# Kernel tuning notes

Measured on AMD Instinct MI355X. Metric: run time of the kernel, lower is better.

The kernel has to match this reference:

```python
import jax, jax.numpy as jnp
import numpy as np

B, S, D_IN = 32, 128, 17
D_PT, D_PAIR, D_OUT = 64, 128, 64
EPS = 1e-5


def _gelu(x):
    return jax.nn.gelu(x, approximate=False)  # torch nn.GELU default (erf)


def _bn(h, g, b):
    # BatchNorm1d (training mode): stats over batch and pair dims, per channel
    mean = h.mean(axis=(0, 1))
    var = h.var(axis=(0, 1))  # biased, matching torch normalization
    return (h - mean) * jax.lax.rsqrt(var + EPS) * g + b


def setup_inputs() -> dict:
    key = jax.random.key(0)
    ks = jax.random.split(key, 8)
    s = lambda k, shp, fan: jax.random.normal(k, shp, jnp.float32) * (1.0 / np.sqrt(fan))
    return {
        "x": jax.random.normal(ks[0], (B, S, D_IN), jnp.float32),
        # pointwise MLP: 17 -> 64 -> 64
        "w1": s(ks[1], (D_IN, D_PT), D_IN), "b1": jnp.zeros((D_PT,), jnp.float32),
        "w2": s(ks[2], (D_PT, D_PT), D_PT), "b2": jnp.zeros((D_PT,), jnp.float32),
        # pair MLP: 128 -> 128 -> 128 (input = 2 * D_PT)
        "wp1": s(ks[3], (2 * D_PT, D_PAIR), 2 * D_PT), "bp1": jnp.zeros((D_PAIR,), jnp.float32),
        "wp2": s(ks[4], (D_PAIR, D_PAIR), D_PAIR), "bp2": jnp.zeros((D_PAIR,), jnp.float32),
        # embed: BN(128) -> Conv1d(128,64,1) -> BN(64) -> GELU -> Conv1d(64,64,1) -> BN(64)
        "g0": jnp.ones((D_PAIR,), jnp.float32), "be0": jnp.zeros((D_PAIR,), jnp.float32),
        "wc1": s(ks[5], (D_PAIR, D_OUT), D_PAIR), "bc1": jnp.zeros((D_OUT,), jnp.float32),
        "g1": jnp.ones((D_OUT,), jnp.float32), "be1": jnp.zeros((D_OUT,), jnp.float32),
        "wc2": s(ks[6], (D_OUT, D_OUT), D_OUT), "bc2": jnp.zeros((D_OUT,), jnp.float32),
        "g2": jnp.ones((D_OUT,), jnp.float32), "be2": jnp.zeros((D_OUT,), jnp.float32),
    }


def reference(x, w1, b1, w2, b2, wp1, bp1, wp2, bp2,
              g0, be0, wc1, bc1, g1, be1, wc2, bc2, g2, be2):
    seq_len = x.shape[1]
    # pointwise MLP
    h = _gelu(x @ w1 + b1)
    h = _gelu(h @ w2 + b2)  # [B, S, D_PT]
    # tril pair gather (xi = features of particle j, xj = of particle i,
    # matching x_rep[b, a, c] = x[b, c] semantics in the torch code)
    i_idx, j_idx = jnp.tril_indices(seq_len)
    xi = h[:, j_idx, :]  # [B, P, D_PT]
    xj = h[:, i_idx, :]
    xij = jnp.concatenate([xi, xj], axis=-1)  # [B, P, 2*D_PT]
    # pair MLP
    e = _gelu(xij @ wp1 + bp1)
    e = _gelu(e @ wp2 + bp2)  # [B, P, D_PAIR]
    # embed stack (Conv1d k=1 == channel-wise linear)
    e = _bn(e, g0, be0)
    e = _gelu(_bn(e @ wc1 + bc1, g1, be1))
    e = _bn(e @ wc2 + bc2, g2, be2)  # [B, P, D_OUT]
    # symmetric scatter into dense pairwise output
    y = jnp.zeros((x.shape[0], seq_len, seq_len, e.shape[-1]), e.dtype)
    y = y.at[:, i_idx, j_idx, :].set(e)
    y = y.at[:, j_idx, i_idx, :].set(e)
    return y
```

## Files before the change

kernel.cpp:

```cpp
#include <hip/hip_runtime.h>
#include <hip/hip_bf16.h>
#include <math.h>

#define BB 32
#define SS 128
#define DIN 17
#define DPT 64
#define DPA 128
#define DOU 64
#define NP 8256
#define NROWS (BB * NP)
#define NCHUNK (NROWS / 128)
#define EPSF 1e-5f

typedef __hip_bfloat16 bf16;
typedef __attribute__((ext_vector_type(8))) short short8;
typedef __attribute__((ext_vector_type(16))) float f32x16;
typedef __attribute__((ext_vector_type(4))) float f32x4;
typedef __attribute__((ext_vector_type(4))) unsigned int uint4v;

#define MFMA32(a, b, c) __builtin_amdgcn_mfma_f32_32x32x16_bf16(a, b, c, 0, 0, 0)

__device__ __forceinline__ float bf2f(short u) {
    return __builtin_bit_cast(float, ((unsigned int)(unsigned short)u) << 16);
}

__device__ __forceinline__ void plswap(unsigned int& a, unsigned int& b) {
    asm("v_permlane32_swap_b32 %0, %1" : "+v"(a), "+v"(b));
}
__device__ __forceinline__ unsigned int cvtpk(float lo, float hi) {
    unsigned int r;
    asm("v_cvt_pk_bf16_f32 %0, %1, %2" : "=v"(r) : "v"(lo), "v"(hi));
    return r;
}

__device__ __forceinline__ void xform(const f32x16& a, short8& o0, short8& o1) {
    unsigned int w[8];
#pragma unroll
    for (int j = 0; j < 8; ++j) w[j] = cvtpk(a[2 * j], a[2 * j + 1]);
    plswap(w[0], w[2]);
    plswap(w[1], w[3]);
    plswap(w[4], w[6]);
    plswap(w[5], w[7]);
    uint4v u0 = {w[0], w[1], w[2], w[3]};
    uint4v u1 = {w[4], w[5], w[6], w[7]};
    o0 = __builtin_bit_cast(short8, u0);
    o1 = __builtin_bit_cast(short8, u1);
}

__device__ __forceinline__ float gelu_exact(float x) {
    float x2 = x * x;
    float m = fmaf(0.0356774081f, x2, 0.7978845608f);
    float e = __expf(2.0f * x * m);
    float r = __builtin_amdgcn_rcpf(e + 1.0f);
    return fmaf(-x, r, x);
}
__device__ __forceinline__ void gelu16(f32x16& a) {
#pragma unroll
    for (int r = 0; r < 16; ++r) a[r] = gelu_exact(a[r]);
}

__global__ void k_pairs(int* __restrict__ pairIJ) {
    int p = blockIdx.x * blockDim.x + threadIdx.x;
    if (p >= NP) return;
    int i = (int)((sqrtf(8.0f * (float)p + 1.0f) - 1.0f) * 0.5f);
    while ((i * (i + 1)) / 2 > p) --i;
    while (((i + 1) * (i + 2)) / 2 <= p) ++i;
    int j = p - (i * (i + 1)) / 2;
    pairIJ[p] = (i << 8) | j;
}

__global__ void k_pack(const float* __restrict__ wp2, const float* __restrict__ wc2,
                       bf16* __restrict__ fragP2, bf16* __restrict__ fragC2) {
    int id = blockIdx.x * 256 + threadIdx.x;
    if (id < 16384) {
        int f = id >> 9, lane = (id >> 3) & 63, i = id & 7;
        int mt = f >> 3, s = f & 7;
        int k = s * 16 + (lane >> 5) * 8 + i;
        int m = mt * 32 + (lane & 31);
        fragP2[id] = __float2bfloat16(wp2[k * DPA + m]);
    } else if (id < 20480) {
        int rem = id - 16384;
        int f = rem >> 9, lane = (rem >> 3) & 63, i = rem & 7;
        int mt = f >> 2, s = f & 3;
        int k = s * 16 + (lane >> 5) * 8 + i;
        int m = mt * 32 + (lane & 31);
        fragC2[rem] = __float2bfloat16(wc2[k * DOU + m]);
    }
}

__global__ void k_fold(const float* __restrict__ a0, const float* __restrict__ d0,
                       const float* __restrict__ wc1, const float* __restrict__ bc1,
                       bf16* __restrict__ fragC1, float* __restrict__ bc1p) {
    int id = blockIdx.x * 256 + threadIdx.x;
    if (id < 8192) {
        int f = id >> 9, lane = (id >> 3) & 63, i = id & 7;
        int mt = f >> 3, s = f & 7;
        int k = s * 16 + (lane >> 5) * 8 + i;
        int m = mt * 32 + (lane & 31);
        fragC1[id] = __float2bfloat16(a0[k] * wc1[k * DOU + m]);
    } else if (id < 8192 + 64) {
        int c = id - 8192;
        float s = bc1[c];
        for (int k = 0; k < DPA; ++k) s = fmaf(d0[k], wc1[k * DOU + c], s);
        bc1p[c] = s;
    }
}

__global__ __launch_bounds__(256) void k_h(
    const float* __restrict__ x, const float* __restrict__ w1,
    const float* __restrict__ b1, const float* __restrict__ w2,
    const float* __restrict__ b2, const float* __restrict__ wp1,
    const float* __restrict__ bp1, bf16* __restrict__ u, bf16* __restrict__ v) {
    __shared__ float h1[4][DPT];
    __shared__ float h2[4][DPT];
    __shared__ float wt[128][64];
    int t = threadIdx.x;
    int rs = t >> 6, c = t & 63;
    int r = blockIdx.x * 4 + rs;
    const float* xr = x + (size_t)r * DIN;
    float acc = b1[c];
#pragma unroll
    for (int k = 0; k < DIN; ++k) acc += xr[k] * w1[k * DPT + c];
    h1[rs][c] = gelu_exact(acc);
    __syncthreads();
    float acc2 = b2[c];
#pragma unroll
    for (int k = 0; k < DPT; ++k) acc2 += h1[rs][k] * w2[k * DPT + c];
    h2[rs][c] = gelu_exact(acc2);

    for (int cp = 0; cp < 2; ++cp) {
        __syncthreads();
        for (int idx = t; idx < 8192; idx += 256) {
            int k = idx >> 6, cc = idx & 63;
            wt[k][cc] = wp1[k * DPA + cp * 64 + cc];
        }
        __syncthreads();
        float au = bp1[cp * 64 + c], av = 0.f;
#pragma unroll
        for (int k = 0; k < 64; ++k) {
            float hk = h2[rs][k];
            au = fmaf(hk, wt[k][c], au);
            av = fmaf(hk, wt[64 + k][c], av);
        }
        u[(size_t)r * DPA + cp * 64 + c] = __float2bfloat16(au);
        v[(size_t)r * DPA + cp * 64 + c] = __float2bfloat16(av);
    }
}

__global__ __launch_bounds__(256, 3) void k_e0m(
    const bf16* __restrict__ u, const bf16* __restrict__ v,
    const int* __restrict__ pairIJ, const short8* __restrict__ fragP2,
    const float* __restrict__ bp2, bf16* __restrict__ e0,
    float* __restrict__ part) {
    __shared__ __align__(16) char lds[32768];
    int t = threadIdx.x;
    int w = t >> 6, l = t & 63;
    int l31 = l & 31, lhi = l >> 5;
    int row0 = blockIdx.x * 128;
    int prow = w * 32 + l31;

    for (int uq = t; uq < 2048; uq += 256)
        *(short8*)(lds + uq * 16) = fragP2[uq];

    int n = row0 + prow;
    int b = n / NP, p = n - b * NP;
    int ij = pairIJ[p];
    const bf16* ur = u + (((size_t)(b * SS + (ij & 255))) << 7);
    const bf16* vr = v + (((size_t)(b * SS + (ij >> 8))) << 7);
    short8 B2[8];
#pragma unroll
    for (int s = 0; s < 8; ++s) {
        short8 us = *(const short8*)(ur + s * 16 + lhi * 8);
        short8 vs = *(const short8*)(vr + s * 16 + lhi * 8);
        float g[8];
#pragma unroll
        for (int i = 0; i < 8; ++i)
            g[i] = gelu_exact(bf2f(us[i]) + bf2f(vs[i]));
        uint4v pk = {cvtpk(g[0], g[1]), cvtpk(g[2], g[3]),
                     cvtpk(g[4], g[5]), cvtpk(g[6], g[7])};
        B2[s] = __builtin_bit_cast(short8, pk);
    }
    __syncthreads();

    short8 o[8];
#pragma unroll
    for (int mp = 0; mp < 2; ++mp) {
        f32x16 c0, c1;
#pragma unroll
        for (int g = 0; g < 4; ++g) {
            f32x4 v0 = *(const f32x4*)(bp2 + (2 * mp) * 32 + g * 8 + lhi * 4);
            f32x4 v1 = *(const f32x4*)(bp2 + (2 * mp + 1) * 32 + g * 8 + lhi * 4);
#pragma unroll
            for (int j = 0; j < 4; ++j) { c0[g * 4 + j] = v0[j]; c1[g * 4 + j] = v1[j]; }
        }
#pragma unroll
        for (int s = 0; s < 8; ++s) {
            short8 a0 = *(const short8*)(lds + (((2 * mp) * 8 + s) * 64 + l) * 16);
            short8 a1 = *(const short8*)(lds + (((2 * mp + 1) * 8 + s) * 64 + l) * 16);
            c0 = MFMA32(a0, B2[s], c0);
            c1 = MFMA32(a1, B2[s], c1);
        }
        gelu16(c0);
        xform(c0, o[4 * mp + 0], o[4 * mp + 1]);
        gelu16(c1);
        xform(c1, o[4 * mp + 2], o[4 * mp + 3]);
    }
    __syncthreads();

    char* stg = lds + w * 8192;
#pragma unroll
    for (int mt = 0; mt < 4; ++mt) {
        int slot0 = 4 * mt + lhi, slot1 = 4 * mt + 2 + lhi;
        *(short8*)(stg + l31 * 256 + ((slot0 * 16) ^ ((l31 & 15) << 4))) = o[2 * mt];
        *(short8*)(stg + l31 * 256 + ((slot1 * 16) ^ ((l31 & 15) << 4))) = o[2 * mt + 1];
    }

    float sum[8], sq[8];
#pragma unroll
    for (int i = 0; i < 8; ++i) { sum[i] = 0.f; sq[i] = 0.f; }
    int slot = l & 15;
#pragma unroll
    for (int q = 0; q < 8; ++q) {
        int r = (l >> 4) + 4 * q;
        short8 vv = *(const short8*)(stg + r * 256 + ((slot * 16) ^ ((r & 15) << 4)));
        *(short8*)(e0 + (size_t)(row0 + w * 32 + r) * DPA + slot * 8) = vv;
#pragma unroll
        for (int i = 0; i < 8; ++i) {
            float f = bf2f(vv[i]);
            sum[i] += f;
            sq[i] += f * f;
        }
    }

    float* sb = (float*)stg;
#pragma unroll
    for (int i = 0; i < 8; ++i) {
        sb[l * 17 + i] = sum[i];
        sb[l * 17 + 8 + i] = sq[i];
    }
    __syncthreads();

    {
        int c = t & 127, isq = t >> 7;
        float s = 0.f;
#pragma unroll
        for (int wv = 0; wv < 4; ++wv) {
            const float* sv = (const float*)(lds + wv * 8192);
#pragma unroll
            for (int g = 0; g < 4; ++g)
                s += sv[(g * 16 + (c >> 3)) * 17 + isq * 8 + (c & 7)];
        }
        part[(size_t)blockIdx.x * 256 + t] = s;
    }
}

__global__ void k_stats(const float* __restrict__ part, int nch, int nblk,
                        float* __restrict__ a, float* __restrict__ d,
                        const float* __restrict__ g, const float* __restrict__ be) {
    int c = blockIdx.x;
    __shared__ float ssum[256], ssq[256];
    float s = 0.f, q = 0.f;
    for (int bidx = threadIdx.x; bidx < nblk; bidx += 256) {
        s += part[(size_t)bidx * (2 * nch) + c];
        q += part[(size_t)bidx * (2 * nch) + nch + c];
    }
    ssum[threadIdx.x] = s;
    ssq[threadIdx.x] = q;
    __syncthreads();
    for (int w = 128; w > 0; w >>= 1) {
        if ((int)threadIdx.x < w) {
            ssum[threadIdx.x] += ssum[threadIdx.x + w];
            ssq[threadIdx.x] += ssq[threadIdx.x + w];
        }
        __syncthreads();
    }
    if (threadIdx.x == 0) {
        float mean = ssum[0] / (float)NROWS;
        float var = ssq[0] / (float)NROWS - mean * mean;
        float rstd = rsqrtf(var + EPSF);
        float aa = g[c] * rstd;
        a[c] = aa;
        d[c] = be[c] - mean * aa;
    }
}

__global__ __launch_bounds__(256) void k_e1m(
    const bf16* __restrict__ e0, const short8* __restrict__ fragC1,
    const float* __restrict__ bc1p, bf16* __restrict__ e1,
    float* __restrict__ part) {
    __shared__ __align__(16) char buf[16384];
    int t = threadIdx.x;
    int w = t >> 6, l = t & 63;
    int l31 = l & 31, lhi = l >> 5;
    int row0 = blockIdx.x * 128;
    int prow = w * 32 + l31;

    short8 Wc[16];
#pragma unroll
    for (int i = 0; i < 16; ++i) Wc[i] = fragC1[i * 64 + l];
    short8 B[8];
#pragma unroll
    for (int s = 0; s < 8; ++s)
        B[s] = *(const short8*)(e0 + (size_t)(row0 + prow) * DPA + s * 16 + lhi * 8);

    f32x16 acc[2];
#pragma unroll
    for (int mt = 0; mt < 2; ++mt)
#pragma unroll
        for (int g = 0; g < 4; ++g) {
            f32x4 bv = *(const f32x4*)(bc1p + mt * 32 + g * 8 + lhi * 4);
#pragma unroll
            for (int j = 0; j < 4; ++j) acc[mt][g * 4 + j] = bv[j];
        }
#pragma unroll
    for (int s = 0; s < 8; ++s) {
        acc[0] = MFMA32(Wc[s], B[s], acc[0]);
        acc[1] = MFMA32(Wc[8 + s], B[s], acc[1]);
    }

#pragma unroll
    for (int mt = 0; mt < 2; ++mt) {
        short8 o0, o1;
        xform(acc[mt], o0, o1);
        int slot0 = 4 * mt + lhi, slot1 = 4 * mt + 2 + lhi;
        *(short8*)(buf + prow * 128 + ((slot0 * 16) ^ ((prow & 7) << 4))) = o0;
        *(short8*)(buf + prow * 128 + ((slot1 * 16) ^ ((prow & 7) << 4))) = o1;
    }
    __syncthreads();

    float sum[8], sq[8];
#pragma unroll
    for (int i = 0; i < 8; ++i) { sum[i] = 0.f; sq[i] = 0.f; }
    int slot = t & 7;
#pragma unroll
    for (int q = 0; q < 4; ++q) {
        int rr = (t >> 3) + 32 * q;
        short8 v = *(const short8*)(buf + rr * 128 + ((slot * 16) ^ ((rr & 7) << 4)));
        *(short8*)(e1 + (size_t)(row0 + rr) * DOU + slot * 8) = v;
#pragma unroll
        for (int i = 0; i < 8; ++i) {
            float f = bf2f(v[i]);
            sum[i] += f;
            sq[i] += f * f;
        }
    }
    __syncthreads();
    float* bb = (float*)buf;
#pragma unroll
    for (int i = 0; i < 8; ++i) {
        bb[t * 16 + i] = sum[i];
        bb[t * 16 + 8 + i] = sq[i];
    }
    __syncthreads();
    if (t < 128) {
        int c = t & 63, isq = t >> 6;
        float s = 0.f;
#pragma unroll
        for (int g = 0; g < 32; ++g)
            s += bb[((c >> 3) + 8 * g) * 16 + isq * 8 + (c & 7)];
        part[(size_t)blockIdx.x * 128 + t] = s;
    }
}

__global__ __launch_bounds__(256) void k_e2m(
    const bf16* __restrict__ e1, const float* __restrict__ a1,
    const float* __restrict__ d1, const short8* __restrict__ fragC2,
    const float* __restrict__ bc2, bf16* __restrict__ e2,
    float* __restrict__ part) {
    __shared__ __align__(16) char buf[16384];
    int t = threadIdx.x;
    int w = t >> 6, l = t & 63;
    int l31 = l & 31, lhi = l >> 5;
    int row0 = blockIdx.x * 128;
    int prow = w * 32 + l31;

    short8 Wc[8];
#pragma unroll
    for (int s = 0; s < 8; ++s) Wc[s] = fragC2[s * 64 + l];

    short8 B[4];
#pragma unroll
    for (int s = 0; s < 4; ++s) {
        short8 raw = *(const short8*)(e1 + (size_t)(row0 + prow) * DOU + s * 16 + lhi * 8);
        int c0 = s * 16 + lhi * 8;
        f32x4 av0 = *(const f32x4*)(a1 + c0), av1 = *(const f32x4*)(a1 + c0 + 4);
        f32x4 dv0 = *(const f32x4*)(d1 + c0), dv1 = *(const f32x4*)(d1 + c0 + 4);
        float gg[8];
#pragma unroll
        for (int i = 0; i < 4; ++i) gg[i] = gelu_exact(fmaf(bf2f(raw[i]), av0[i], dv0[i]));
#pragma unroll
        for (int i = 0; i < 4; ++i) gg[4 + i] = gelu_exact(fmaf(bf2f(raw[4 + i]), av1[i], dv1[i]));
        uint4v uu = {cvtpk(gg[0], gg[1]), cvtpk(gg[2], gg[3]),
                     cvtpk(gg[4], gg[5]), cvtpk(gg[6], gg[7])};
        B[s] = __builtin_bit_cast(short8, uu);
    }

    f32x16 acc[2];
#pragma unroll
    for (int mt = 0; mt < 2; ++mt)
#pragma unroll
        for (int g = 0; g < 4; ++g) {
            f32x4 bv = *(const f32x4*)(bc2 + mt * 32 + g * 8 + lhi * 4);
#pragma unroll
            for (int j = 0; j < 4; ++j) acc[mt][g * 4 + j] = bv[j];
        }
#pragma unroll
    for (int s = 0; s < 4; ++s) {
        acc[0] = MFMA32(Wc[s], B[s], acc[0]);
        acc[1] = MFMA32(Wc[4 + s], B[s], acc[1]);
    }

#pragma unroll
    for (int mt = 0; mt < 2; ++mt) {
        short8 o0, o1;
        xform(acc[mt], o0, o1);
        int slot0 = 4 * mt + lhi, slot1 = 4 * mt + 2 + lhi;
        *(short8*)(buf + prow * 128 + ((slot0 * 16) ^ ((prow & 7) << 4))) = o0;
        *(short8*)(buf + prow * 128 + ((slot1 * 16) ^ ((prow & 7) << 4))) = o1;
    }
    __syncthreads();

    float sum[8], sq[8];
#pragma unroll
    for (int i = 0; i < 8; ++i) { sum[i] = 0.f; sq[i] = 0.f; }
    int slot = t & 7;
#pragma unroll
    for (int q = 0; q < 4; ++q) {
        int rr = (t >> 3) + 32 * q;
        short8 v = *(const short8*)(buf + rr * 128 + ((slot * 16) ^ ((rr & 7) << 4)));
        *(short8*)(e2 + (size_t)(row0 + rr) * DOU + slot * 8) = v;
#pragma unroll
        for (int i = 0; i < 8; ++i) {
            float f = bf2f(v[i]);
            sum[i] += f;
            sq[i] += f * f;
        }
    }
    __syncthreads();
    float* bb = (float*)buf;
#pragma unroll
    for (int i = 0; i < 8; ++i) {
        bb[t * 16 + i] = sum[i];
        bb[t * 16 + 8 + i] = sq[i];
    }
    __syncthreads();
    if (t < 128) {
        int c = t & 63, isq = t >> 6;
        float s = 0.f;
#pragma unroll
        for (int g = 0; g < 32; ++g)
            s += bb[((c >> 3) + 8 * g) * 16 + isq * 8 + (c & 7)];
        part[(size_t)blockIdx.x * 128 + t] = s;
    }
}

__global__ void k_out(const bf16* __restrict__ e2, const int* __restrict__ pairIJ,
                      const float* __restrict__ a2, const float* __restrict__ d2,
                      float* __restrict__ y) {
    int t = threadIdx.x;
    int n = blockIdx.x * 32 + (t >> 3);
    int c0 = (t & 7) * 8;
    int b = n / NP, p = n - b * NP;
    int ij = pairIJ[p];
    int ii = ij >> 8, jj = ij & 255;
    short8 raw = *(const short8*)(e2 + (size_t)n * DOU + c0);
    f32x4 aLo = *(const f32x4*)(a2 + c0), aHi = *(const f32x4*)(a2 + c0 + 4);
    f32x4 dLo = *(const f32x4*)(d2 + c0), dHi = *(const f32x4*)(d2 + c0 + 4);
    f32x4 v0, v1;
#pragma unroll
    for (int i = 0; i < 4; ++i) v0[i] = fmaf(bf2f(raw[i]), aLo[i], dLo[i]);
#pragma unroll
    for (int i = 0; i < 4; ++i) v1[i] = fmaf(bf2f(raw[4 + i]), aHi[i], dHi[i]);
    float* y1 = y + ((size_t)(b * SS + ii) * SS + jj) * DOU + c0;
    float* y2 = y + ((size_t)(b * SS + jj) * SS + ii) * DOU + c0;
    *(f32x4*)y1 = v0;
    *(f32x4*)(y1 + 4) = v1;
    *(f32x4*)y2 = v0;
    *(f32x4*)(y2 + 4) = v1;
}

extern "C" void kernel_launch(void* const* d_in, const int* in_sizes, int n_in,
                              void* d_out, int out_size, void* d_ws, size_t ws_size,
                              hipStream_t stream) {
    const float* x   = (const float*)d_in[0];
    const float* w1  = (const float*)d_in[1];
    const float* b1  = (const float*)d_in[2];
    const float* w2  = (const float*)d_in[3];
    const float* b2  = (const float*)d_in[4];
    const float* wp1 = (const float*)d_in[5];
    const float* bp1 = (const float*)d_in[6];
    const float* wp2 = (const float*)d_in[7];
    const float* bp2 = (const float*)d_in[8];
    const float* g0  = (const float*)d_in[9];
    const float* be0 = (const float*)d_in[10];
    const float* wc1 = (const float*)d_in[11];
    const float* bc1 = (const float*)d_in[12];
    const float* g1  = (const float*)d_in[13];
    const float* be1 = (const float*)d_in[14];
    const float* wc2 = (const float*)d_in[15];
    const float* bc2 = (const float*)d_in[16];
    const float* g2  = (const float*)d_in[17];
    const float* be2 = (const float*)d_in[18];

    char* ws = (char*)d_ws;
    const size_t OFF_PAIR   = 0;
    const size_t OFF_PART   = 557568;
    const size_t OFF_FRAGP2 = 2703872;
    const size_t OFF_FRAGC1 = 2736640;
    const size_t OFF_FRAGC2 = 2753024;
    const size_t OFF_BC1P   = 2761216;
    const size_t OFF_A0 = 2761472, OFF_D0 = 2761984;
    const size_t OFF_A1 = 2762496, OFF_D1 = 2762752;
    const size_t OFF_A2 = 2763008, OFF_D2 = 2763264;
    const size_t OFF_E2 = 2763520;

    int*   pairIJ = (int*)(ws + OFF_PAIR);
    float* part   = (float*)(ws + OFF_PART);
    bf16*  fragP2 = (bf16*)(ws + OFF_FRAGP2);
    bf16*  fragC1 = (bf16*)(ws + OFF_FRAGC1);
    bf16*  fragC2 = (bf16*)(ws + OFF_FRAGC2);
    float* bc1p   = (float*)(ws + OFF_BC1P);
    float* a0 = (float*)(ws + OFF_A0);
    float* d0 = (float*)(ws + OFF_D0);
    float* a1 = (float*)(ws + OFF_A1);
    float* d1 = (float*)(ws + OFF_D1);
    float* a2 = (float*)(ws + OFF_A2);
    float* d2 = (float*)(ws + OFF_D2);
    bf16*  e2 = (bf16*)(ws + OFF_E2);

    bf16* e0 = (bf16*)d_out;
    bf16* e1 = (bf16*)((char*)d_out + (size_t)NROWS * DPA * sizeof(bf16));
    bf16* u  = (bf16*)((char*)d_out + 101449728);
    bf16* v  = (bf16*)((char*)d_out + 102498304);
    float* y = (float*)d_out;

    k_pairs<<<(NP + 255) / 256, 256, 0, stream>>>(pairIJ);
    k_pack<<<80, 256, 0, stream>>>(wp2, wc2, fragP2, fragC2);
    k_h<<<(BB * SS) / 4, 256, 0, stream>>>(x, w1, b1, w2, b2, wp1, bp1, u, v);
    k_e0m<<<NCHUNK, 256, 0, stream>>>(u, v, pairIJ, (const short8*)fragP2, bp2, e0, part);
    k_stats<<<DPA, 256, 0, stream>>>(part, DPA, NCHUNK, a0, d0, g0, be0);
    k_fold<<<33, 256, 0, stream>>>(a0, d0, wc1, bc1, fragC1, bc1p);
    k_e1m<<<NCHUNK, 256, 0, stream>>>(e0, (const short8*)fragC1, bc1p, e1, part);
    k_stats<<<DOU, 256, 0, stream>>>(part, DOU, NCHUNK, a1, d1, g1, be1);
    k_e2m<<<NCHUNK, 256, 0, stream>>>(e1, a1, d1, (const short8*)fragC2, bc2, e2, part);
    k_stats<<<DOU, 256, 0, stream>>>(part, DOU, NCHUNK, a2, d2, g2, be2);
    k_out<<<NROWS / 32, 256, 0, stream>>>(e2, pairIJ, a2, d2, y);
}
```

Measured before the change: 173.5 us.

## Make pair-MLP kernel loop over four chunks with prefetch and shuffle-reduced stats

k_e0m now has each block process four 128-row chunks instead of one. The fragP2 weight fragment is loaded into LDS once per four chunks, and the gathered u/v rows for the next chunk are prefetched while the current chunk runs its MFMAs. Per-channel BatchNorm sums are accumulated across chunks in registers and reduced with wave shuffles, so fewer partials are written and k_stats reads 516 blocks instead of 2064. k_h also drops the LDS staging of wp1 and two block barriers in favour of direct global reads. The costs are higher register and LDS use in k_e0m, with occupancy lowered from 3 to 2 blocks, and less parallelism from the smaller grid.

New measurement: 170.1 us. -2.0%, faster.

```diff
diff --git a/kernel.cpp b/kernel.cpp
--- a/kernel.cpp
+++ b/kernel.cpp
@@ -11,6 +11,7 @@
 #define NP 8256
 #define NROWS (BB * NP)
 #define NCHUNK (NROWS / 128)
+#define NBLK0 516
 #define EPSF 1e-5f
 
 typedef __hip_bfloat16 bf16;
@@ -114,7 +115,6 @@
     const float* __restrict__ bp1, bf16* __restrict__ u, bf16* __restrict__ v) {
     __shared__ float h1[4][DPT];
     __shared__ float h2[4][DPT];
-    __shared__ float wt[128][64];
     int t = threadIdx.x;
     int rs = t >> 6, c = t & 63;
     int r = blockIdx.x * 4 + rs;
@@ -123,134 +123,161 @@
 #pragma unroll
     for (int k = 0; k < DIN; ++k) acc += xr[k] * w1[k * DPT + c];
     h1[rs][c] = gelu_exact(acc);
-    __syncthreads();
     float acc2 = b2[c];
 #pragma unroll
     for (int k = 0; k < DPT; ++k) acc2 += h1[rs][k] * w2[k * DPT + c];
     h2[rs][c] = gelu_exact(acc2);
 
+#pragma unroll
     for (int cp = 0; cp < 2; ++cp) {
-        __syncthreads();
-        for (int idx = t; idx < 8192; idx += 256) {
-            int k = idx >> 6, cc = idx & 63;
-            wt[k][cc] = wp1[k * DPA + cp * 64 + cc];
-        }
-        __syncthreads();
         float au = bp1[cp * 64 + c], av = 0.f;
-#pragma unroll
+#pragma unroll 8
         for (int k = 0; k < 64; ++k) {
             float hk = h2[rs][k];
-            au = fmaf(hk, wt[k][c], au);
-            av = fmaf(hk, wt[64 + k][c], av);
+            au = fmaf(hk, wp1[k * DPA + cp * 64 + c], au);
+            av = fmaf(hk, wp1[(64 + k) * DPA + cp * 64 + c], av);
         }
         u[(size_t)r * DPA + cp * 64 + c] = __float2bfloat16(au);
         v[(size_t)r * DPA + cp * 64 + c] = __float2bfloat16(av);
     }
 }
 
-__global__ __launch_bounds__(256, 3) void k_e0m(
+__global__ __launch_bounds__(256, 2) void k_e0m(
     const bf16* __restrict__ u, const bf16* __restrict__ v,
     const int* __restrict__ pairIJ, const short8* __restrict__ fragP2,
     const float* __restrict__ bp2, bf16* __restrict__ e0,
     float* __restrict__ part) {
-    __shared__ __align__(16) char lds[32768];
+    __shared__ __align__(16) char lds[49152];
     int t = threadIdx.x;
     int w = t >> 6, l = t & 63;
     int l31 = l & 31, lhi = l >> 5;
-    int row0 = blockIdx.x * 128;
+    char* stg = lds + 32768 + w * 4096;
     int prow = w * 32 + l31;
 
-    for (int uq = t; uq < 2048; uq += 256)
-        *(short8*)(lds + uq * 16) = fragP2[uq];
-
-    int n = row0 + prow;
-    int b = n / NP, p = n - b * NP;
-    int ij = pairIJ[p];
-    const bf16* ur = u + (((size_t)(b * SS + (ij & 255))) << 7);
-    const bf16* vr = v + (((size_t)(b * SS + (ij >> 8))) << 7);
-    short8 B2[8];
+    int nn = blockIdx.x * 4 * 128 + prow;
+    int bb = nn / NP;
+    int ij = pairIJ[nn - bb * NP];
+
+    for (int q = t; q < 2048; q += 256)
+        *(short8*)(lds + q * 16) = fragP2[q];
+
+    const bf16* ur = u + (((size_t)(bb * SS + (ij & 255))) << 7);
+    const bf16* vr = v + (((size_t)(bb * SS + (ij >> 8))) << 7);
+    short8 pu[8], pv[8];
 #pragma unroll
     for (int s = 0; s < 8; ++s) {
-        short8 us = *(const short8*)(ur + s * 16 + lhi * 8);
-        short8 vs = *(const short8*)(vr + s * 16 + lhi * 8);
-        float g[8];
-#pragma unroll
-        for (int i = 0; i < 8; ++i)
-            g[i] = gelu_exact(bf2f(us[i]) + bf2f(vs[i]));
-        uint4v pk = {cvtpk(g[0], g[1]), cvtpk(g[2], g[3]),
-                     cvtpk(g[4], g[5]), cvtpk(g[6], g[7])};
-        B2[s] = __builtin_bit_cast(short8, pk);
-    }
-    __syncthreads();
-
-    short8 o[8];
-#pragma unroll
-    for (int mp = 0; mp < 2; ++mp) {
-        f32x16 c0, c1;
-#pragma unroll
-        for (int g = 0; g < 4; ++g) {
-            f32x4 v0 = *(const f32x4*)(bp2 + (2 * mp) * 32 + g * 8 + lhi * 4);
-            f32x4 v1 = *(const f32x4*)(bp2 + (2 * mp + 1) * 32 + g * 8 + lhi * 4);
-#pragma unroll
-            for (int j = 0; j < 4; ++j) { c0[g * 4 + j] = v0[j]; c1[g * 4 + j] = v1[j]; }
-        }
+        pu[s] = *(const short8*)(ur + s * 16 + lhi * 8);
+        pv[s] = *(const short8*)(vr + s * 16 + lhi * 8);
+    }
+
+    float sum[16], sq[16];
+#pragma unroll
+    for (int i = 0; i < 16; ++i) { sum[i] = 0.f; sq[i] = 0.f; }
+
+    __syncthreads();
+
+    for (int it = 0; it < 4; ++it) {
+        int ijn = 0, bn = 0;
+        if (it < 3) {
+            int nn2 = nn + 128;
+            bn = nn2 / NP;
+            ijn = pairIJ[nn2 - bn * NP];
+        }
+
+        short8 B2[8];
 #pragma unroll
         for (int s = 0; s < 8; ++s) {
-            short8 a0 = *(const short8*)(lds + (((2 * mp) * 8 + s) * 64 + l) * 16);
-            short8 a1 = *(const short8*)(lds + (((2 * mp + 1) * 8 + s) * 64 + l) * 16);
-            c0 = MFMA32(a0, B2[s], c0);
-            c1 = MFMA32(a1, B2[s], c1);
-        }
-        gelu16(c0);
-        xform(c0, o[4 * mp + 0], o[4 * mp + 1]);
-        gelu16(c1);
-        xform(c1, o[4 * mp + 2], o[4 * mp + 3]);
-    }
-    __syncthreads();
-
-    char* stg = lds + w * 8192;
-#pragma unroll
-    for (int mt = 0; mt < 4; ++mt) {
-        int slot0 = 4 * mt + lhi, slot1 = 4 * mt + 2 + lhi;
-        *(short8*)(stg + l31 * 256 + ((slot0 * 16) ^ ((l31 & 15) << 4))) = o[2 * mt];
-        *(short8*)(stg + l31 * 256 + ((slot1 * 16) ^ ((l31 & 15) << 4))) = o[2 * mt + 1];
-    }
-
-    float sum[8], sq[8];
-#pragma unroll
-    for (int i = 0; i < 8; ++i) { sum[i] = 0.f; sq[i] = 0.f; }
-    int slot = l & 15;
-#pragma unroll
-    for (int q = 0; q < 8; ++q) {
-        int r = (l >> 4) + 4 * q;
-        short8 vv = *(const short8*)(stg + r * 256 + ((slot * 16) ^ ((r & 15) << 4)));
-        *(short8*)(e0 + (size_t)(row0 + w * 32 + r) * DPA + slot * 8) = vv;
+            float g[8];
+#pragma unroll
+            for (int i = 0; i < 8; ++i)
+                g[i] = gelu_exact(bf2f(pu[s][i]) + bf2f(pv[s][i]));
+            uint4v pk = {cvtpk(g[0], g[1]), cvtpk(g[2], g[3]),
+                         cvtpk(g[4], g[5]), cvtpk(g[6], g[7])};
+            B2[s] = __builtin_bit_cast(short8, pk);
+        }
+
+        if (it < 3) {
+            const bf16* urn = u + (((size_t)(bn * SS + (ijn & 255))) << 7);
+            const bf16* vrn = v + (((size_t)(bn * SS + (ijn >> 8))) << 7);
+#pragma unroll
+            for (int s = 0; s < 8; ++s) {
+                pu[s] = *(const short8*)(urn + s * 16 + lhi * 8);
+                pv[s] = *(const short8*)(vrn + s * 16 + lhi * 8);
+            }
+        }
+
+        int rowbase = nn - l31;
+#pragma unroll
+        for (int mp = 0; mp < 2; ++mp) {
+            f32x16 c0, c1;
+#pragma unroll
+            for (int g = 0; g < 4; ++g) {
+                f32x4 v0 = *(const f32x4*)(bp2 + (2 * mp) * 32 + g * 8 + lhi * 4);
+                f32x4 v1 = *(const f32x4*)(bp2 + (2 * mp + 1) * 32 + g * 8 + lhi * 4);
+#pragma unroll
+                for (int j = 0; j < 4; ++j) { c0[g * 4 + j] = v0[j]; c1[g * 4 + j] = v1[j]; }
+            }
+#pragma unroll
+            for (int s = 0; s < 8; ++s) {
+                short8 a0 = *(const short8*)(lds + (((2 * mp) * 8 + s) * 64 + l) * 16);
+                short8 a1 = *(const short8*)(lds + (((2 * mp + 1) * 8 + s) * 64 + l) * 16);
+                c0 = MFMA32(a0, B2[s], c0);
+                c1 = MFMA32(a1, B2[s], c1);
+            }
+            short8 o0, o1, o2, o3;
+            gelu16(c0);
+            xform(c0, o0, o1);
+            gelu16(c1);
+            xform(c1, o2, o3);
+            *(short8*)(stg + l31 * 128 + (((lhi) * 16) ^ ((l31 & 7) << 4))) = o0;
+            *(short8*)(stg + l31 * 128 + (((2 + lhi) * 16) ^ ((l31 & 7) << 4))) = o1;
+            *(short8*)(stg + l31 * 128 + (((4 + lhi) * 16) ^ ((l31 & 7) << 4))) = o2;
+            *(short8*)(stg + l31 * 128 + (((6 + lhi) * 16) ^ ((l31 & 7) << 4))) = o3;
+            int slot = l & 7;
+#pragma unroll
+            for (int q = 0; q < 4; ++q) {
+                int r = (l >> 3) + 8 * q;
+                short8 vv = *(const short8*)(stg + r * 128 +
+                                             ((slot * 16) ^ ((r & 7) << 4)));
+                *(short8*)(e0 + (size_t)(rowbase + r) * DPA + mp * 64 + slot * 8) = vv;
+#pragma unroll
+                for (int i = 0; i < 8; ++i) {
+                    float f = bf2f(vv[i]);
+                    sum[mp * 8 + i] += f;
+                    sq[mp * 8 + i] += f * f;
+                }
+            }
+        }
+        nn += 128;
+    }
+
+#pragma unroll
+    for (int i = 0; i < 16; ++i) {
+        sum[i] += __shfl_xor(sum[i], 8);
+        sum[i] += __shfl_xor(sum[i], 16);
+        sum[i] += __shfl_xor(sum[i], 32);
+        sq[i] += __shfl_xor(sq[i], 8);
+        sq[i] += __shfl_xor(sq[i], 16);
+        sq[i] += __shfl_xor(sq[i], 32);
+    }
+    __syncthreads();
+    float* sb = (float*)lds;
+    if (l < 8) {
 #pragma unroll
         for (int i = 0; i < 8; ++i) {
-            float f = bf2f(vv[i]);
-            sum[i] += f;
-            sq[i] += f * f;
-        }
-    }
-
-    float* sb = (float*)stg;
-#pragma unroll
-    for (int i = 0; i < 8; ++i) {
-        sb[l * 17 + i] = sum[i];
-        sb[l * 17 + 8 + i] = sq[i];
-    }
-    __syncthreads();
-
+            sb[w * 256 + 0 * 64 + l * 8 + i] = sum[i];
+            sb[w * 256 + 1 * 64 + l * 8 + i] = sum[8 + i];
+            sb[w * 256 + 2 * 64 + l * 8 + i] = sq[i];
+            sb[w * 256 + 3 * 64 + l * 8 + i] = sq[8 + i];
+        }
+    }
+    __syncthreads();
     {
         int c = t & 127, isq = t >> 7;
-        float s = 0.f;
-#pragma unroll
-        for (int wv = 0; wv < 4; ++wv) {
-            const float* sv = (const float*)(lds + wv * 8192);
-#pragma unroll
-            for (int g = 0; g < 4; ++g)
-                s += sv[(g * 16 + (c >> 3)) * 17 + isq * 8 + (c & 7)];
-        }
+        int grp = isq * 2 + (c >> 6);
+        int cl = c & 63;
+        float s = sb[0 * 256 + grp * 64 + cl] + sb[1 * 256 + grp * 64 + cl] +
+                  sb[2 * 256 + grp * 64 + cl] + sb[3 * 256 + grp * 64 + cl];
         part[(size_t)blockIdx.x * 256 + t] = s;
     }
 }
@@ -538,8 +565,8 @@
     k_pairs<<<(NP + 255) / 256, 256, 0, stream>>>(pairIJ);
     k_pack<<<80, 256, 0, stream>>>(wp2, wc2, fragP2, fragC2);
     k_h<<<(BB * SS) / 4, 256, 0, stream>>>(x, w1, b1, w2, b2, wp1, bp1, u, v);
-    k_e0m<<<NCHUNK, 256, 0, stream>>>(u, v, pairIJ, (const short8*)fragP2, bp2, e0, part);
-    k_stats<<<DPA, 256, 0, stream>>>(part, DPA, NCHUNK, a0, d0, g0, be0);
+    k_e0m<<<NBLK0, 256, 0, stream>>>(u, v, pairIJ, (const short8*)fragP2, bp2, e0, part);
+    k_stats<<<DPA, 256, 0, stream>>>(part, DPA, NBLK0, a0, d0, g0, be0);
     k_fold<<<33, 256, 0, stream>>>(a0, d0, wc1, bc1, fragC1, bc1p);
     k_e1m<<<NCHUNK, 256, 0, stream>>>(e0, (const short8*)fragC1, bc1p, e1, part);
     k_stats<<<DOU, 256, 0, stream>>>(part, DOU, NCHUNK, a1, d1, g1, be1);
```
